# Optimization experiments

Measured on AMD Instinct MI355X. Metric: run time of the kernel, lower is better.

The kernel has to match this reference:

```python
import jax, jax.numpy as jnp
import numpy as np

N_NODES = 10000
N_EDGES = 320000
F_NODE = 16
NUM_BESSEL = 8
M = 32           # env_embed_multiplicity
LAT = 128        # latent dimension
R_MAX = 5.0
P_CUT = 6.0      # polynomial cutoff order
AVG_NEIGH = 32.0
SQRT3 = 1.7320508075688772
SQRT2 = 1.4142135623730951


def _mlp(x, weights):
    # nequip ScalarMLPFunction: linear layers with 1/sqrt(fan_in) norm, silu between layers
    h = x
    n = len(weights)
    for i, W in enumerate(weights):
        h = h @ W * (1.0 / np.sqrt(W.shape[0]))
        if i < n - 1:
            h = jax.nn.silu(h)
    return h


def _weight_channels(Y, w):
    # MakeWeightedChannels: Y [E,4] = (0e | 1e), w [E,M,2] per-irrep weights -> [E,M,4]
    return jnp.concatenate([w[..., 0:1] * Y[:, None, 0:1],
                            w[..., 1:2] * Y[:, None, 1:4]], axis=-1)


def setup_inputs():
    key = jax.random.key(0)
    ks = jax.random.split(key, 16)

    def w(k, i, o):
        return jax.random.normal(k, (i, o), jnp.float32)

    two_body_in = 2 * F_NODE + NUM_BESSEL  # 40
    return {
        "coordinates": jax.random.uniform(ks[0], (N_NODES, 3), jnp.float32),
        "node_attrs": jax.random.uniform(ks[1], (N_NODES, F_NODE), jnp.float32),
        "edge_index": jax.random.randint(ks[2], (2, N_EDGES), 0, N_NODES),
        "W2b0": w(ks[3], two_body_in, 64),
        "W2b1": w(ks[4], 64, 128),
        "W2b2": w(ks[5], 128, LAT),
        "Wenv0": w(ks[6], LAT, 4 * M),       # initial-edge embed + env weights (2 irreps each)
        "Wlat0": w(ks[7], LAT + 2 * M, 128),
        "Wlat1": w(ks[8], 128, LAT),
        "Ws0": w(ks[9], 2 * M, M),            # e3nn Linear, scalar block (2 paths)
        "Wv0": w(ks[10], 3 * M, M),           # e3nn Linear, vector block (3 paths)
        "Wenv1": w(ks[11], LAT, 2 * M),
        "Wfin0": w(ks[12], LAT + 2 * M, 128),
        "Wfin1": w(ks[13], 128, LAT),
    }


def reference(coordinates, node_attrs, edge_index, W2b0, W2b1, W2b2, Wenv0,
              Wlat0, Wlat1, Ws0, Wv0, Wenv1, Wfin0, Wfin1):
    sender, center = edge_index[0], edge_index[1]
    vec = coordinates[center] - coordinates[sender]            # [E,3]
    r = jnp.sqrt(jnp.sum(vec * vec, axis=-1) + 1e-12)          # [E]
    u = r / R_MAX
    p = P_CUT
    fcut = (1.0 - (p + 1.0) * (p + 2.0) / 2.0 * u**p
            + p * (p + 2.0) * u**(p + 1.0)
            - p * (p + 1.0) / 2.0 * u**(p + 2.0))
    fcut = jnp.where(u < 1.0, fcut, 0.0)
    n = jnp.arange(1, NUM_BESSEL + 1, dtype=jnp.float32)
    bessel = np.sqrt(2.0 / R_MAX) * jnp.sin(n * jnp.pi * u[:, None]) / r[:, None]
    edge_feats = bessel * fcut[:, None]                        # [E,8]
    unit = vec / r[:, None]
    Y = jnp.concatenate([jnp.ones_like(r)[:, None], SQRT3 * unit], axis=-1)  # [E,4] component-normalized SH

    inv_sqrt_n = 1.0 / np.sqrt(AVG_NEIGH)
    E = r.shape[0]

    # two-body latent (layer 0)
    lat_in = jnp.concatenate([node_attrs[center], node_attrs[sender], edge_feats], -1)
    lat = _mlp(lat_in, (W2b0, W2b1, W2b2)) * fcut[:, None]     # [E,LAT]
    w_all = lat @ Wenv0 * (1.0 / np.sqrt(LAT))                 # [E,4M]
    w_edge = w_all[:, :2 * M].reshape(E, M, 2)
    w_env = w_all[:, 2 * M:].reshape(E, M, 2)
    feat = _weight_channels(Y, w_edge)                         # [E,M,4] initial edge embed
    env = jax.ops.segment_sum(_weight_channels(Y, w_env), center, num_segments=N_NODES)
    env = env[center] * inv_sqrt_n                             # [E,M,4]

    fs, fv = feat[..., 0], feat[..., 1:]
    es, ev = env[..., 0], env[..., 1:]
    # layer-0 tensor product instruction list (uuu, no weights)
    p0 = fs * es                               # 0e x 0e -> 0e
    p1 = jnp.sum(fv * ev, -1) / SQRT3          # 1e x 1e -> 0e
    p2 = fs[..., None] * ev                    # 0e x 1e -> 1e
    p3 = fv * es[..., None]                    # 1e x 0e -> 1e
    p4 = jnp.cross(fv, ev) / SQRT2             # 1e x 1e -> 1e
    scal0 = jnp.concatenate([p0, p1], -1)      # [E,2M] scalar outs (n_scalar_outs=2)
    # per-layer e3nn Linear
    s_mix = scal0 @ Ws0 * (1.0 / np.sqrt(2 * M))                         # [E,M]
    v_mix = jnp.einsum('eic,io->eoc', jnp.concatenate([p2, p3, p4], 1), Wv0) * (1.0 / np.sqrt(3 * M))  # [E,M,3]

    # latent resnet update (update param 0 -> sigmoid = 0.5)
    alpha = 0.5
    c_old = 1.0 / np.sqrt(alpha * alpha + 1.0)
    c_new = alpha * c_old
    new_lat = _mlp(jnp.concatenate([lat, scal0], -1), (Wlat0, Wlat1)) * fcut[:, None]
    lat = c_old * lat + c_new * new_lat

    # layer 1 env embedding + tensor product (last layer -> scalars only)
    w_env1 = (lat @ Wenv1 * (1.0 / np.sqrt(LAT))).reshape(E, M, 2)
    env1 = jax.ops.segment_sum(_weight_channels(Y, w_env1), center, num_segments=N_NODES)
    env1 = env1[center] * inv_sqrt_n
    q0 = s_mix * env1[..., 0]
    q1 = jnp.sum(v_mix * env1[..., 1:], -1) / SQRT3
    scal1 = jnp.concatenate([q0, q1], -1)      # [E,2M]

    new_lat = _mlp(jnp.concatenate([lat, scal1], -1), (Wfin0, Wfin1)) * fcut[:, None]
    lat = c_old * lat + c_new * new_lat

    node_out = jax.ops.segment_sum(lat, center, num_segments=N_NODES) * inv_sqrt_n
    return node_out
```

## Files before the change

kernel.cpp:

```cpp
#include <hip/hip_runtime.h>
#include <hip/hip_bf16.h>
#include <math.h>

typedef __hip_bfloat16 bf16;
typedef unsigned short us;
typedef __attribute__((ext_vector_type(8))) short short8;
typedef __attribute__((ext_vector_type(4))) float floatx4;

#define EPI_SPLIT    1
#define EPI_STORE    2
#define EPI_RESID    4

#define INV_SQRT_N 0.17677669529663687f
#define INV_SQRT3  0.5773502691896258f
#define INV_SQRT2  0.7071067811865476f
#define C_OLD      0.8944271909999159f
#define C_NEW      0.4472135954999579f
#define PI_F       3.14159265358979323846f
#define SQRT3_F    1.7320508075688772f
#define BESSEL_PREF 0.6324555320336759f

__device__ __forceinline__ float b2f(bf16 x) { return __bfloat162float(x); }
__device__ __forceinline__ bf16  f2b(float x) { return __float2bfloat16(x); }
__device__ __forceinline__ us f2bu(float x) {
  bf16 h = f2b(x); us u; __builtin_memcpy(&u, &h, 2); return u;
}
__device__ __forceinline__ float silu_f(float v) { return v / (1.f + __expf(-v)); }
__device__ __forceinline__ floatx4 mfma16(short8 a, short8 b, floatx4 c) {
  return __builtin_amdgcn_mfma_f32_16x16x32_bf16(a, b, c, 0, 0, 0);
}
__device__ __forceinline__ short8 ld8(const void* p) {
  return *reinterpret_cast<const short8*>(p);
}
#define ZERO8 ((short8){0,0,0,0,0,0,0,0})

__global__ __launch_bounds__(256) void k_deg(
    const int* __restrict__ eidx, int E, int* __restrict__ deg) {
  int e = blockIdx.x * 256 + threadIdx.x;
  if (e < E) atomicAdd(&deg[eidx[E + e]], 1);
}

__global__ __launch_bounds__(1024) void k_scan(
    const int* __restrict__ deg, int N,
    int* __restrict__ rowptr, int* __restrict__ cursor) {
  __shared__ int part[1024];
  int t = threadIdx.x;
  int C = (N + 1023) / 1024;
  int base = t * C;
  int s = 0;
  for (int i = 0; i < C; ++i) { int idx = base + i; if (idx < N) s += deg[idx]; }
  part[t] = s;
  __syncthreads();
  for (int off = 1; off < 1024; off <<= 1) {
    int v = (t >= off) ? part[t - off] : 0;
    __syncthreads();
    part[t] += v;
    __syncthreads();
  }
  int excl = (t == 0) ? 0 : part[t - 1];
  for (int i = 0; i < C; ++i) {
    int idx = base + i;
    if (idx < N) { rowptr[idx] = excl; cursor[idx] = excl; excl += deg[idx]; }
  }
  if (t == 0) rowptr[N] = part[1023];
}

__global__ __launch_bounds__(256) void k_fill(
    const int* __restrict__ eidx, int E, int* __restrict__ cursor,
    int* __restrict__ eord, int* __restrict__ cent) {
  int e = blockIdx.x * 256 + threadIdx.x;
  if (e >= E) return;
  int c = eidx[E + e];
  int slot = atomicAdd(&cursor[c], 1);
  eord[slot] = e;
  cent[slot] = c;
}

__global__ __launch_bounds__(256) void k_geom(
    const float* __restrict__ coords, const float* __restrict__ nattr,
    const int* __restrict__ eidx, const int* __restrict__ eord, int E,
    float* __restrict__ fcut, float* __restrict__ Yb, bf16* __restrict__ a64) {
  int j = blockIdx.x * 256 + threadIdx.x;
  if (j >= E) return;
  int e = eord[j];
  int s = eidx[e], c = eidx[E + e];
  float dx = coords[c*3+0] - coords[s*3+0];
  float dy = coords[c*3+1] - coords[s*3+1];
  float dz = coords[c*3+2] - coords[s*3+2];
  float r = sqrtf(dx*dx + dy*dy + dz*dz + 1e-12f);
  float u = r * 0.2f;
  float u3 = u*u*u;
  float u6 = u3*u3, u7 = u6*u, u8 = u7*u;
  float fc = 1.f - 28.f*u6 + 48.f*u7 - 21.f*u8;
  fc = (u < 1.f) ? fc : 0.f;
  float inv_r = 1.f / r;
  fcut[j] = fc;
  Yb[j*4+0] = 1.f;
  Yb[j*4+1] = SQRT3_F * dx * inv_r;
  Yb[j*4+2] = SQRT3_F * dy * inv_r;
  Yb[j*4+3] = SQRT3_F * dz * inv_r;
  bf16* row = a64 + (long)j * 64;
  #pragma unroll
  for (int i = 0; i < 16; ++i) row[i]      = f2b(nattr[(long)c*16 + i]);
  #pragma unroll
  for (int i = 0; i < 16; ++i) row[16 + i] = f2b(nattr[(long)s*16 + i]);
  float pref = BESSEL_PREF * inv_r * fc;
  #pragma unroll
  for (int n = 1; n <= 8; ++n)
    row[32 + n - 1] = f2b(pref * sinf((float)n * PI_F * u));
  #pragma unroll
  for (int i = 40; i < 64; ++i) row[i] = f2b(0.f);
}

__device__ __forceinline__ void wp(const float* W, us* Wt, int K, int NOUT, int t) {
  int n = t / K, k = t % K;
  Wt[n * K + k] = f2bu(W[k * NOUT + n]);
}

__global__ __launch_bounds__(256) void k_wprep_all(
    const float* W2b0, const float* W2b1, const float* W2b2,
    const float* Wenv0, const float* Wlat0, const float* Wlat1,
    const float* Wenv1, const float* Wfin0, const float* Wfin1,
    const float* Ws0, const float* Wv0,
    us* W2b0p, us* W2b1t, us* W2b2t, us* Wenv0t, us* Wlat0t, us* Wlat1t,
    us* Wenv1t, us* Wfin0t, us* Wfin1t, us* Wmixt) {
  int t = blockIdx.x * 256 + threadIdx.x;
  if (t < 8192)  { wp(W2b1,  W2b1t,  64, 128, t); return; } t -= 8192;
  if (t < 16384) { wp(W2b2,  W2b2t, 128, 128, t); return; } t -= 16384;
  if (t < 16384) { wp(Wenv0, Wenv0t,128, 128, t); return; } t -= 16384;
  if (t < 24576) { wp(Wlat0, Wlat0t,192, 128, t); return; } t -= 24576;
  if (t < 16384) { wp(Wlat1, Wlat1t,128, 128, t); return; } t -= 16384;
  if (t < 8192)  { wp(Wenv1, Wenv1t,128,  64, t); return; } t -= 8192;
  if (t < 24576) { wp(Wfin0, Wfin0t,192, 128, t); return; } t -= 24576;
  if (t < 16384) { wp(Wfin1, Wfin1t,128, 128, t); return; } t -= 16384;
  if (t < 4096)  {
    int n = t >> 6, k = t & 63;
    W2b0p[n * 64 + k] = (k < 40) ? f2bu(W2b0[k * 64 + n]) : 0;
    return;
  } t -= 4096;
  if (t < 5120) {
    int o = t / 160, k = t % 160;
    float v = (k < 64) ? Ws0[k * 32 + o] : Wv0[(k - 64) * 32 + o];
    Wmixt[o * 160 + k] = f2bu(v);
  }
}

__global__ __launch_bounds__(256) void k_envg(
    const bf16* __restrict__ wenv, const float* __restrict__ Yb,
    const int* __restrict__ rowptr, int N, float* __restrict__ env) {
  int t = blockIdx.x * 256 + threadIdx.x;
  if (t >= N * 32) return;
  int n = t >> 5, m = t & 31;
  int j0 = rowptr[n], j1 = rowptr[n + 1];
  float a0 = 0.f, a1 = 0.f, a2 = 0.f, a3 = 0.f;
  for (int j = j0; j < j1; ++j) {
    float w0 = b2f(wenv[(long)j*64 + 2*m]);
    float w1 = b2f(wenv[(long)j*64 + 2*m + 1]);
    float4 y = *reinterpret_cast<const float4*>(&Yb[(long)j*4]);
    a0 += w0;
    a1 += w1 * y.y;
    a2 += w1 * y.z;
    a3 += w1 * y.w;
  }
  *reinterpret_cast<float4*>(&env[(long)n*128 + m*4]) = make_float4(a0, a1, a2, a3);
}

__global__ __launch_bounds__(256) void k_nodeg(
    const bf16* __restrict__ lat, const int* __restrict__ rowptr,
    int N, float* __restrict__ out) {
  int t = blockIdx.x * 256 + threadIdx.x;
  if (t >= N * 128) return;
  int n = t >> 7, j = t & 127;
  int j0 = rowptr[n], j1 = rowptr[n + 1];
  float s = 0.f;
  for (int q = j0; q < j1; ++q)
    s += b2f(lat[(long)q*128 + j]);
  out[t] = s * INV_SQRT_N;
}

template<int NOUT, int EPI>
__global__ __launch_bounds__(256) void mgemm(
    const bf16* __restrict__ A, const us* __restrict__ Wt,
    bf16* __restrict__ out1, bf16* __restrict__ out2, float scale, int E) {
  constexpr int K = 128, KP = 136, NC = 4;
  constexpr int CT = NOUT / 64;
  __shared__ __align__(16) us As[64 * KP];
  int tid = threadIdx.x;
  int lane = tid & 63, w = tid >> 6;
  int nl = lane & 15, quad = lane >> 4;
  long e0 = (long)blockIdx.x * 64;

  short8 wf[NC][CT];
  #pragma unroll
  for (int kc = 0; kc < NC; ++kc)
    #pragma unroll
    for (int ct = 0; ct < CT; ++ct)
      wf[kc][ct] = ld8(Wt + (long)(w*CT*16 + ct*16 + nl) * K + kc*32 + quad*8);

  #pragma unroll
  for (int it = 0; it < 4; ++it) {
    int i = tid + it * 256;
    int row = i >> 4, col = (i & 15) * 8;
    long eg = e0 + row;
    short8 v = (eg < E) ? ld8(A + eg * 128 + col) : ZERO8;
    *(short8*)&As[row * KP + col] = v;
  }
  __syncthreads();

  floatx4 acc[4][CT];
  #pragma unroll
  for (int i = 0; i < 4; ++i)
    #pragma unroll
    for (int j = 0; j < CT; ++j) acc[i][j] = (floatx4){0.f,0.f,0.f,0.f};
  #pragma unroll
  for (int kc = 0; kc < NC; ++kc) {
    short8 af[4];
    #pragma unroll
    for (int et = 0; et < 4; ++et)
      af[et] = ld8(&As[(et*16 + nl) * KP + kc*32 + quad*8]);
    #pragma unroll
    for (int et = 0; et < 4; ++et)
      #pragma unroll
      for (int ct = 0; ct < CT; ++ct)
        acc[et][ct] = mfma16(af[et], wf[kc][ct], acc[et][ct]);
  }

  #pragma unroll
  for (int et = 0; et < 4; ++et)
    #pragma unroll
    for (int ct = 0; ct < CT; ++ct)
      #pragma unroll
      for (int r = 0; r < 4; ++r) {
        long eg = e0 + et*16 + quad*4 + r;
        if (eg >= E) continue;
        int col = w*CT*16 + ct*16 + nl;
        float v = acc[et][ct][r] * scale;
        if constexpr (EPI == EPI_SPLIT) {
          if (col < 64) out1[eg * 64 + col] = f2b(v);
          else          out2[eg * 64 + (col - 64)] = f2b(v);
        } else {
          out1[eg * NOUT + col] = f2b(v);
        }
      }
}

__global__ __launch_bounds__(256) void mfused3(
    const bf16* __restrict__ a64, const us* __restrict__ W0p,
    const us* __restrict__ W1t, const us* __restrict__ W2t,
    bf16* __restrict__ lat, const float* __restrict__ fcut,
    float s40, float s64s, float s128, int E) {
  constexpr int AP = 72, HP = 136;
  __shared__ __align__(16) us SB[64 * 144];
  us* As = SB;
  us* H0 = SB + 64 * AP;
  us* Hs = SB;
  int tid = threadIdx.x;
  int lane = tid & 63, w = tid >> 6;
  int nl = lane & 15, quad = lane >> 4;
  long e0 = (long)blockIdx.x * 64;

  short8 w0f[2], w1f[2][2], w2f[4][2];
  #pragma unroll
  for (int kc = 0; kc < 2; ++kc)
    w0f[kc] = ld8(W0p + (w*16 + nl) * 64 + kc*32 + quad*8);
  #pragma unroll
  for (int kc = 0; kc < 2; ++kc)
    #pragma unroll
    for (int ct = 0; ct < 2; ++ct)
      w1f[kc][ct] = ld8(W1t + (long)(w*32 + ct*16 + nl) * 64 + kc*32 + quad*8);
  #pragma unroll
  for (int kc = 0; kc < 4; ++kc)
    #pragma unroll
    for (int ct = 0; ct < 2; ++ct)
      w2f[kc][ct] = ld8(W2t + (long)(w*32 + ct*16 + nl) * 128 + kc*32 + quad*8);

  #pragma unroll
  for (int it = 0; it < 2; ++it) {
    int i = tid + it * 256;
    int row = i >> 3, col = (i & 7) * 8;
    long eg = e0 + row;
    short8 v = (eg < E) ? ld8(a64 + eg * 64 + col) : ZERO8;
    *(short8*)&As[row * AP + col] = v;
  }
  __syncthreads();

  floatx4 a0[4];
  #pragma unroll
  for (int i = 0; i < 4; ++i) a0[i] = (floatx4){0.f,0.f,0.f,0.f};
  #pragma unroll
  for (int kc = 0; kc < 2; ++kc) {
    short8 af[4];
    #pragma unroll
    for (int et = 0; et < 4; ++et)
      af[et] = ld8(&As[(et*16 + nl) * AP + kc*32 + quad*8]);
    #pragma unroll
    for (int et = 0; et < 4; ++et) a0[et] = mfma16(af[et], w0f[kc], a0[et]);
  }
  #pragma unroll
  for (int et = 0; et < 4; ++et)
    #pragma unroll
    for (int r = 0; r < 4; ++r)
      H0[(et*16 + quad*4 + r) * AP + w*16 + nl] = f2bu(silu_f(a0[et][r] * s40));
  __syncthreads();

  floatx4 acc[4][2];
  #pragma unroll
  for (int i = 0; i < 4; ++i)
    #pragma unroll
    for (int j = 0; j < 2; ++j) acc[i][j] = (floatx4){0.f,0.f,0.f,0.f};
  #pragma unroll
  for (int kc = 0; kc < 2; ++kc) {
    short8 af[4];
    #pragma unroll
    for (int et = 0; et < 4; ++et)
      af[et] = ld8(&H0[(et*16 + nl) * AP + kc*32 + quad*8]);
    #pragma unroll
    for (int et = 0; et < 4; ++et)
      #pragma unroll
      for (int ct = 0; ct < 2; ++ct)
        acc[et][ct] = mfma16(af[et], w1f[kc][ct], acc[et][ct]);
  }
  __syncthreads();

  #pragma unroll
  for (int et = 0; et < 4; ++et)
    #pragma unroll
    for (int ct = 0; ct < 2; ++ct)
      #pragma unroll
      for (int r = 0; r < 4; ++r)
        Hs[(et*16 + quad*4 + r) * HP + w*32 + ct*16 + nl] =
            f2bu(silu_f(acc[et][ct][r] * s64s));
  __syncthreads();

  #pragma unroll
  for (int i = 0; i < 4; ++i)
    #pragma unroll
    for (int j = 0; j < 2; ++j) acc[i][j] = (floatx4){0.f,0.f,0.f,0.f};
  #pragma unroll
  for (int kc = 0; kc < 4; ++kc) {
    short8 af[4];
    #pragma unroll
    for (int et = 0; et < 4; ++et)
      af[et] = ld8(&Hs[(et*16 + nl) * HP + kc*32 + quad*8]);
    #pragma unroll
    for (int et = 0; et < 4; ++et)
      #pragma unroll
      for (int ct = 0; ct < 2; ++ct)
        acc[et][ct] = mfma16(af[et], w2f[kc][ct], acc[et][ct]);
  }
  #pragma unroll
  for (int et = 0; et < 4; ++et)
    #pragma unroll
    for (int ct = 0; ct < 2; ++ct)
      #pragma unroll
      for (int r = 0; r < 4; ++r) {
        long eg = e0 + et*16 + quad*4 + r;
        if (eg >= E) continue;
        lat[eg * 128 + w*32 + ct*16 + nl] =
            f2b(acc[et][ct][r] * s128 * fcut[eg]);
      }
}

template<int EPI>
__global__ __launch_bounds__(256) void mfused(
    const bf16* __restrict__ A, const bf16* __restrict__ A2,
    const us* __restrict__ W0t, const us* __restrict__ W1t,
    bf16* __restrict__ outb, const float* __restrict__ fcut,
    float scale0, float scale1, int E) {
  constexpr int K = 192, KP = 200, NC0 = 6, HP = 136;
  __shared__ __align__(16) us SB[64 * KP];
  us* As = SB;
  us* Hs = SB;
  int tid = threadIdx.x;
  int lane = tid & 63, w = tid >> 6;
  int nl = lane & 15, quad = lane >> 4;
  long e0 = (long)blockIdx.x * 64;

  short8 w0f[NC0][2];
  #pragma unroll
  for (int kc = 0; kc < NC0; ++kc)
    #pragma unroll
    for (int ct = 0; ct < 2; ++ct)
      w0f[kc][ct] = ld8(W0t + (long)(w*32 + ct*16 + nl) * K + kc*32 + quad*8);

  #pragma unroll
  for (int it = 0; it < 4; ++it) {
    int i = tid + it * 256;
    int row = i >> 4, col = (i & 15) * 8;
    long eg = e0 + row;
    short8 v = (eg < E) ? ld8(A + eg * 128 + col) : ZERO8;
    *(short8*)&As[row * KP + col] = v;
  }
  #pragma unroll
  for (int it = 0; it < 2; ++it) {
    int i = tid + it * 256;
    int row = i >> 3, col = (i & 7) * 8;
    long eg = e0 + row;
    short8 v = (eg < E) ? ld8(A2 + eg * 64 + col) : ZERO8;
    *(short8*)&As[row * KP + 128 + col] = v;
  }
  __syncthreads();

  floatx4 acc[4][2];
  #pragma unroll
  for (int i = 0; i < 4; ++i)
    #pragma unroll
    for (int j = 0; j < 2; ++j) acc[i][j] = (floatx4){0.f,0.f,0.f,0.f};
  #pragma unroll
  for (int kc = 0; kc < NC0; ++kc) {
    short8 af[4];
    #pragma unroll
    for (int et = 0; et < 4; ++et)
      af[et] = ld8(&As[(et*16 + nl) * KP + kc*32 + quad*8]);
    #pragma unroll
    for (int et = 0; et < 4; ++et)
      #pragma unroll
      for (int ct = 0; ct < 2; ++ct)
        acc[et][ct] = mfma16(af[et], w0f[kc][ct], acc[et][ct]);
  }

  short8 w1f[4][2];
  #pragma unroll
  for (int kc = 0; kc < 4; ++kc)
    #pragma unroll
    for (int ct = 0; ct < 2; ++ct)
      w1f[kc][ct] = ld8(W1t + (long)(w*32 + ct*16 + nl) * 128 + kc*32 + quad*8);

  __syncthreads();

  #pragma unroll
  for (int et = 0; et < 4; ++et)
    #pragma unroll
    for (int ct = 0; ct < 2; ++ct)
      #pragma unroll
      for (int r = 0; r < 4; ++r)
        Hs[(et*16 + quad*4 + r) * HP + w*32 + ct*16 + nl] =
            f2bu(silu_f(acc[et][ct][r] * scale0));
  __syncthreads();

  #pragma unroll
  for (int i = 0; i < 4; ++i)
    #pragma unroll
    for (int j = 0; j < 2; ++j) acc[i][j] = (floatx4){0.f,0.f,0.f,0.f};
  #pragma unroll
  for (int kc = 0; kc < 4; ++kc) {
    short8 af[4];
    #pragma unroll
    for (int et = 0; et < 4; ++et)
      af[et] = ld8(&Hs[(et*16 + nl) * HP + kc*32 + quad*8]);
    #pragma unroll
    for (int et = 0; et < 4; ++et)
      #pragma unroll
      for (int ct = 0; ct < 2; ++ct)
        acc[et][ct] = mfma16(af[et], w1f[kc][ct], acc[et][ct]);
  }

  #pragma unroll
  for (int et = 0; et < 4; ++et)
    #pragma unroll
    for (int ct = 0; ct < 2; ++ct)
      #pragma unroll
      for (int r = 0; r < 4; ++r) {
        long eg = e0 + et*16 + quad*4 + r;
        if (eg >= E) continue;
        int col = w*32 + ct*16 + nl;
        float v = acc[et][ct][r] * scale1 * fcut[eg];
        long idx = eg * 128 + col;
        outb[idx] = f2b(C_OLD * b2f(outb[idx]) + C_NEW * v);
      }
}

__global__ __launch_bounds__(256) void k_prod(
    const bf16* __restrict__ wedge, const float* __restrict__ env,
    const float* __restrict__ Yb, const int* __restrict__ cent, int E,
    bf16* __restrict__ scal) {
  long t = (long)blockIdx.x * 256 + threadIdx.x;
  if (t >= (long)E * 32) return;
  long e = t >> 5;
  int m = (int)(t & 31);
  int c = cent[e];
  float w0 = b2f(wedge[e*64 + 2*m]), w1 = b2f(wedge[e*64 + 2*m + 1]);
  const float* ep = env + (long)c*128 + m*4;
  float es  = ep[0] * INV_SQRT_N;
  float evx = ep[1] * INV_SQRT_N, evy = ep[2] * INV_SQRT_N, evz = ep[3] * INV_SQRT_N;
  float y1 = Yb[e*4+1], y2 = Yb[e*4+2], y3 = Yb[e*4+3];
  float fvx = w1*y1, fvy = w1*y2, fvz = w1*y3;
  scal[e*64 + m]      = f2b(w0 * es);
  scal[e*64 + 32 + m] = f2b((fvx*evx + fvy*evy + fvz*evz) * INV_SQRT3);
}

__global__ __launch_bounds__(256) void k_mix2(
    const bf16* __restrict__ wedge, const float* __restrict__ env,
    const float* __restrict__ env1, const float* __restrict__ Yb,
    const int* __restrict__ cent, const us* __restrict__ Wm,
    int E, bf16* __restrict__ scal) {
  constexpr int PP = 360;
  constexpr int RP = 132;
  __shared__ __align__(16) unsigned char SB[64 * PP * 2];
  __shared__ __align__(16) us Wl[32 * 160];
  us* P = (us*)SB;
  float* R = (float*)SB;
  int tid = threadIdx.x;
  int lane = tid & 63, w = tid >> 6;
  int nl = lane & 15, quad = lane >> 4;
  long e0 = (long)blockIdx.x * 64;

  for (int i = tid; i < 640; i += 256)
    *(short8*)&Wl[i * 8] = ld8(Wm + i * 8);

  int m = tid & 31;
  #pragma unroll
  for (int it = 0; it < 8; ++it) {
    int el = (tid >> 5) + it * 8;
    long e = e0 + el;
    if (e < E) {
      int c = cent[e];
      float w0 = b2f(wedge[e*64 + 2*m]), w1 = b2f(wedge[e*64 + 2*m + 1]);
      float4 ev4 = *(const float4*)(env + (long)c*128 + m*4);
      float4 y   = *(const float4*)(Yb + e*4);
      float es  = ev4.x * INV_SQRT_N;
      float evx = ev4.y * INV_SQRT_N, evy = ev4.z * INV_SQRT_N, evz = ev4.w * INV_SQRT_N;
      float fvx = w1*y.y, fvy = w1*y.z, fvz = w1*y.w;
      us* p = P + el * PP;
      p[m]       = f2bu(w0 * es);
      p[32 + m]  = f2bu((fvx*evx + fvy*evy + fvz*evz) * INV_SQRT3);
      p[64 + m]  = f2bu(w0 * evx);
      p[96 + m]  = f2bu(fvx * es);
      p[128 + m] = f2bu((fvy*evz - fvz*evy) * INV_SQRT2);
      p[160 + m] = f2bu(w0 * evy);
      p[192 + m] = f2bu(fvy * es);
      p[224 + m] = f2bu((fvz*evx - fvx*evz) * INV_SQRT2);
      p[256 + m] = f2bu(w0 * evz);
      p[288 + m] = f2bu(fvz * es);
      p[320 + m] = f2bu((fvx*evy - fvy*evx) * INV_SQRT2);
    } else {
      us* p = P + el * PP;
      #pragma unroll
      for (int q = 0; q < 11; ++q) p[q*32 + m] = 0;
    }
  }
  __syncthreads();

  floatx4 acc[4][2];
  #pragma unroll
  for (int i = 0; i < 4; ++i)
    #pragma unroll
    for (int j = 0; j < 2; ++j) acc[i][j] = (floatx4){0.f,0.f,0.f,0.f};
  int pbase  = (w == 0) ? 0 : 64 + (w - 1) * 96;
  int wkbase = (w == 0) ? 0 : 64;
  int ksteps = (w == 0) ? 2 : 3;
  for (int ks = 0; ks < ksteps; ++ks) {
    short8 af[4], bv[2];
    #pragma unroll
    for (int et = 0; et < 4; ++et)
      af[et] = ld8(&P[(et*16 + nl) * PP + pbase + ks*32 + quad*8]);
    #pragma unroll
    for (int ct = 0; ct < 2; ++ct)
      bv[ct] = ld8(&Wl[(ct*16 + nl) * 160 + wkbase + ks*32 + quad*8]);
    #pragma unroll
    for (int et = 0; et < 4; ++et)
      #pragma unroll
      for (int ct = 0; ct < 2; ++ct)
        acc[et][ct] = mfma16(af[et], bv[ct], acc[et][ct]);
  }
  __syncthreads();

  #pragma unroll
  for (int et = 0; et < 4; ++et)
    #pragma unroll
    for (int ct = 0; ct < 2; ++ct)
      #pragma unroll
      for (int r = 0; r < 4; ++r) {
        int el = et*16 + quad*4 + r;
        R[el * RP + w*32 + ct*16 + nl] = acc[et][ct][r];
      }
  __syncthreads();

  #pragma unroll
  for (int it = 0; it < 8; ++it) {
    int el = (tid >> 5) + it * 8;
    long e = e0 + el;
    if (e >= E) continue;
    int o = m;
    int c = cent[e];
    float4 e1 = *(const float4*)(env1 + (long)c*128 + o*4);
    float sr = R[el * RP + o];
    float vx = R[el * RP + 32 + o];
    float vy = R[el * RP + 64 + o];
    float vz = R[el * RP + 96 + o];
    float q0 = sr * 0.125f * (e1.x * INV_SQRT_N);
    float q1 = (vx*e1.y + vy*e1.z + vz*e1.w) *
               (0.10206207261596577f * INV_SQRT_N * INV_SQRT3);
    scal[e*64 + o]      = f2b(q0);
    scal[e*64 + 32 + o] = f2b(q1);
  }
}

extern "C" void kernel_launch(void* const* d_in, const int* in_sizes, int n_in,
                              void* d_out, int out_size, void* d_ws, size_t ws_size,
                              hipStream_t stream) {
  const float* coords = (const float*)d_in[0];
  const float* nattr  = (const float*)d_in[1];
  const int*   eidx   = (const int*)d_in[2];
  const float* W2b0   = (const float*)d_in[3];
  const float* W2b1   = (const float*)d_in[4];
  const float* W2b2   = (const float*)d_in[5];
  const float* Wenv0  = (const float*)d_in[6];
  const float* Wlat0  = (const float*)d_in[7];
  const float* Wlat1  = (const float*)d_in[8];
  const float* Ws0    = (const float*)d_in[9];
  const float* Wv0    = (const float*)d_in[10];
  const float* Wenv1  = (const float*)d_in[11];
  const float* Wfin0  = (const float*)d_in[12];
  const float* Wfin1  = (const float*)d_in[13];
  float* out = (float*)d_out;
  int E = in_sizes[2] / 2;
  int N = in_sizes[0] / 3;

  float* fcut   = (float*)d_ws;
  float* Yb     = fcut + (size_t)E;
  float* env    = Yb + (size_t)E*4;
  float* env1   = env + (size_t)N*128;
  int*   deg    = (int*)(env1 + (size_t)N*128);
  int*   rowptr = deg + N;
  int*   cursor = rowptr + (N + 8);
  int*   eord   = cursor + N;
  int*   cent   = eord + E;
  bf16*  b64    = (bf16*)(cent + E);
  bf16*  lat    = b64 + (size_t)E*64;
  bf16*  S      = lat + (size_t)E*128;
  us* W2b1t  = (us*)(S + (size_t)E*64);
  us* W2b2t  = W2b1t + 128*64;
  us* Wenv0t = W2b2t + 128*128;
  us* Wlat0t = Wenv0t + 128*128;
  us* Wlat1t = Wlat0t + 128*192;
  us* Wenv1t = Wlat1t + 128*128;
  us* Wfin0t = Wenv1t + 64*128;
  us* Wfin1t = Wfin0t + 128*192;
  us* W2b0p  = Wfin1t + 128*128;
  us* Wmixt  = W2b0p + 64*64;

  hipMemsetAsync(deg, 0, (size_t)N * sizeof(int), stream);

  dim3 blk(256);
  const float s40  = 0.15811388300841897f;
  const float s64  = 0.125f;
  const float s128 = 0.08838834764831845f;
  const float s192 = 0.07216878364870323f;
  int gB = (E + 63) / 64;
  int gE = (E + 255) / 256;

  k_deg<<<gE, blk, 0, stream>>>(eidx, E, deg);
  k_scan<<<1, 1024, 0, stream>>>(deg, N, rowptr, cursor);
  k_fill<<<gE, blk, 0, stream>>>(eidx, E, cursor, eord, cent);
  k_geom<<<gE, blk, 0, stream>>>(coords, nattr, eidx, eord, E, fcut, Yb, S );
  k_wprep_all<<<dim3(548), blk, 0, stream>>>(
      W2b0, W2b1, W2b2, Wenv0, Wlat0, Wlat1, Wenv1, Wfin0, Wfin1, Ws0, Wv0,
      W2b0p, W2b1t, W2b2t, Wenv0t, Wlat0t, Wlat1t, Wenv1t, Wfin0t, Wfin1t, Wmixt);

  mfused3<<<gB, blk, 0, stream>>>(
      S , W2b0p, W2b1t, W2b2t, lat, fcut, s40, s64, s128, E);

  mgemm<128,EPI_SPLIT><<<gB, blk, 0, stream>>>(
      lat, Wenv0t, b64, S , s128, E);

  k_envg<<<dim3((N*32 + 255) / 256), blk, 0, stream>>>(
      S , Yb, rowptr, N, env);

  k_prod<<<dim3((int)(((long)E*32 + 255) / 256)), blk, 0, stream>>>(
      b64, env, Yb, cent, E, S );

  mfused<EPI_RESID><<<gB, blk, 0, stream>>>(
      lat, S , Wlat0t, Wlat1t, lat, fcut, s192, s128, E);

  mgemm<64,EPI_STORE><<<gB, blk, 0, stream>>>(
      lat, Wenv1t, S , nullptr, s128, E);

  k_envg<<<dim3((N*32 + 255) / 256), blk, 0, stream>>>(
      S , Yb, rowptr, N, env1);

  k_mix2<<<gB, blk, 0, stream>>>(
      b64, env, env1, Yb, cent, Wmixt, E, S );

  mfused<EPI_RESID><<<gB, blk, 0, stream>>>(
      lat, S , Wfin0t, Wfin1t, lat, fcut, s192, s128, E);

  k_nodeg<<<dim3((N*128 + 255) / 256), blk, 0, stream>>>(
      lat, rowptr, N, out);
}
```

Baseline: 771.5 us.

## Fuse env-weight GEMMs into MLP kernels and env gather with product

Folds the Wenv0 projection into the two-body MLP kernel and the Wenv1 projection into the first latent-update kernel. The freshly computed latent tile is staged in shared memory and multiplied in place, so the separate GEMM kernels and their re-read of the latent array go away. The env gather and the per-edge product are merged into one node-ordered kernel that computes the product right after the segment sum. This removes the scattered cent-indexed env reads and two launches, at the cost of extra register pressure, extra syncs and a serial per-node loop in the merged gather.

```diff
diff --git a/kernel.cpp b/kernel.cpp
--- a/kernel.cpp
+++ b/kernel.cpp
@@ -6,10 +6,6 @@
 typedef unsigned short us;
 typedef __attribute__((ext_vector_type(8))) short short8;
 typedef __attribute__((ext_vector_type(4))) float floatx4;
-
-#define EPI_SPLIT    1
-#define EPI_STORE    2
-#define EPI_RESID    4
 
 #define INV_SQRT_N 0.17677669529663687f
 #define INV_SQRT3  0.5773502691896258f
@@ -24,6 +20,9 @@
 __device__ __forceinline__ bf16  f2b(float x) { return __float2bfloat16(x); }
 __device__ __forceinline__ us f2bu(float x) {
   bf16 h = f2b(x); us u; __builtin_memcpy(&u, &h, 2); return u;
+}
+__device__ __forceinline__ float bu2f(us u) {
+  bf16 h; __builtin_memcpy(&h, &u, 2); return b2f(h);
 }
 __device__ __forceinline__ float silu_f(float v) { return v / (1.f + __expf(-v)); }
 __device__ __forceinline__ floatx4 mfma16(short8 a, short8 b, floatx4 c) {
@@ -145,6 +144,37 @@
   }
 }
 
+__global__ __launch_bounds__(256) void k_envgp(
+    const bf16* __restrict__ wenv, const bf16* __restrict__ wedge,
+    const float* __restrict__ Yb, const int* __restrict__ rowptr,
+    int N, float* __restrict__ env, bf16* __restrict__ scal) {
+  int t = blockIdx.x * 256 + threadIdx.x;
+  if (t >= N * 32) return;
+  int n = t >> 5, m = t & 31;
+  int j0 = rowptr[n], j1 = rowptr[n + 1];
+  float a0 = 0.f, a1 = 0.f, a2 = 0.f, a3 = 0.f;
+  for (int j = j0; j < j1; ++j) {
+    float w0 = b2f(wenv[(long)j*64 + 2*m]);
+    float w1 = b2f(wenv[(long)j*64 + 2*m + 1]);
+    float4 y = *reinterpret_cast<const float4*>(&Yb[(long)j*4]);
+    a0 += w0;
+    a1 += w1 * y.y;
+    a2 += w1 * y.z;
+    a3 += w1 * y.w;
+  }
+  *reinterpret_cast<float4*>(&env[(long)n*128 + m*4]) = make_float4(a0, a1, a2, a3);
+  float es  = a0 * INV_SQRT_N;
+  float evx = a1 * INV_SQRT_N, evy = a2 * INV_SQRT_N, evz = a3 * INV_SQRT_N;
+  for (int j = j0; j < j1; ++j) {
+    float w0 = b2f(wedge[(long)j*64 + 2*m]);
+    float w1 = b2f(wedge[(long)j*64 + 2*m + 1]);
+    float4 y = *reinterpret_cast<const float4*>(&Yb[(long)j*4]);
+    float fvx = w1*y.y, fvy = w1*y.z, fvz = w1*y.w;
+    scal[(long)j*64 + m]      = f2b(w0 * es);
+    scal[(long)j*64 + 32 + m] = f2b((fvx*evx + fvy*evy + fvz*evz) * INV_SQRT3);
+  }
+}
+
 __global__ __launch_bounds__(256) void k_envg(
     const bf16* __restrict__ wenv, const float* __restrict__ Yb,
     const int* __restrict__ rowptr, int N, float* __restrict__ env) {
@@ -178,76 +208,12 @@
   out[t] = s * INV_SQRT_N;
 }
 
-template<int NOUT, int EPI>
-__global__ __launch_bounds__(256) void mgemm(
-    const bf16* __restrict__ A, const us* __restrict__ Wt,
-    bf16* __restrict__ out1, bf16* __restrict__ out2, float scale, int E) {
-  constexpr int K = 128, KP = 136, NC = 4;
-  constexpr int CT = NOUT / 64;
-  __shared__ __align__(16) us As[64 * KP];
-  int tid = threadIdx.x;
-  int lane = tid & 63, w = tid >> 6;
-  int nl = lane & 15, quad = lane >> 4;
-  long e0 = (long)blockIdx.x * 64;
-
-  short8 wf[NC][CT];
-  #pragma unroll
-  for (int kc = 0; kc < NC; ++kc)
-    #pragma unroll
-    for (int ct = 0; ct < CT; ++ct)
-      wf[kc][ct] = ld8(Wt + (long)(w*CT*16 + ct*16 + nl) * K + kc*32 + quad*8);
-
-  #pragma unroll
-  for (int it = 0; it < 4; ++it) {
-    int i = tid + it * 256;
-    int row = i >> 4, col = (i & 15) * 8;
-    long eg = e0 + row;
-    short8 v = (eg < E) ? ld8(A + eg * 128 + col) : ZERO8;
-    *(short8*)&As[row * KP + col] = v;
-  }
-  __syncthreads();
-
-  floatx4 acc[4][CT];
-  #pragma unroll
-  for (int i = 0; i < 4; ++i)
-    #pragma unroll
-    for (int j = 0; j < CT; ++j) acc[i][j] = (floatx4){0.f,0.f,0.f,0.f};
-  #pragma unroll
-  for (int kc = 0; kc < NC; ++kc) {
-    short8 af[4];
-    #pragma unroll
-    for (int et = 0; et < 4; ++et)
-      af[et] = ld8(&As[(et*16 + nl) * KP + kc*32 + quad*8]);
-    #pragma unroll
-    for (int et = 0; et < 4; ++et)
-      #pragma unroll
-      for (int ct = 0; ct < CT; ++ct)
-        acc[et][ct] = mfma16(af[et], wf[kc][ct], acc[et][ct]);
-  }
-
-  #pragma unroll
-  for (int et = 0; et < 4; ++et)
-    #pragma unroll
-    for (int ct = 0; ct < CT; ++ct)
-      #pragma unroll
-      for (int r = 0; r < 4; ++r) {
-        long eg = e0 + et*16 + quad*4 + r;
-        if (eg >= E) continue;
-        int col = w*CT*16 + ct*16 + nl;
-        float v = acc[et][ct][r] * scale;
-        if constexpr (EPI == EPI_SPLIT) {
-          if (col < 64) out1[eg * 64 + col] = f2b(v);
-          else          out2[eg * 64 + (col - 64)] = f2b(v);
-        } else {
-          out1[eg * NOUT + col] = f2b(v);
-        }
-      }
-}
-
-__global__ __launch_bounds__(256) void mfused3(
+__global__ __launch_bounds__(256) void mfused3s(
     const bf16* __restrict__ a64, const us* __restrict__ W0p,
     const us* __restrict__ W1t, const us* __restrict__ W2t,
-    bf16* __restrict__ lat, const float* __restrict__ fcut,
+    const us* __restrict__ Wenv0t,
+    bf16* __restrict__ lat, bf16* __restrict__ b64, bf16* __restrict__ wenv,
+    const float* __restrict__ fcut,
     float s40, float s64s, float s128, int E) {
   constexpr int AP = 72, HP = 136;
   __shared__ __align__(16) us SB[64 * 144];
@@ -348,6 +314,49 @@
       for (int ct = 0; ct < 2; ++ct)
         acc[et][ct] = mfma16(af[et], w2f[kc][ct], acc[et][ct]);
   }
+
+  short8 wef[4][2];
+  #pragma unroll
+  for (int kc = 0; kc < 4; ++kc)
+    #pragma unroll
+    for (int ct = 0; ct < 2; ++ct)
+      wef[kc][ct] = ld8(Wenv0t + (long)(w*32 + ct*16 + nl) * 128 + kc*32 + quad*8);
+
+  __syncthreads();
+
+  #pragma unroll
+  for (int et = 0; et < 4; ++et)
+    #pragma unroll
+    for (int ct = 0; ct < 2; ++ct)
+      #pragma unroll
+      for (int r = 0; r < 4; ++r) {
+        long eg = e0 + et*16 + quad*4 + r;
+        int col = w*32 + ct*16 + nl;
+        us lv = 0;
+        if (eg < E) {
+          lv = f2bu(acc[et][ct][r] * s128 * fcut[eg]);
+          lat[eg * 128 + col] = f2b(bu2f(lv));
+        }
+        Hs[(et*16 + quad*4 + r) * HP + col] = lv;
+      }
+  __syncthreads();
+
+  #pragma unroll
+  for (int i = 0; i < 4; ++i)
+    #pragma unroll
+    for (int j = 0; j < 2; ++j) acc[i][j] = (floatx4){0.f,0.f,0.f,0.f};
+  #pragma unroll
+  for (int kc = 0; kc < 4; ++kc) {
+    short8 af[4];
+    #pragma unroll
+    for (int et = 0; et < 4; ++et)
+      af[et] = ld8(&Hs[(et*16 + nl) * HP + kc*32 + quad*8]);
+    #pragma unroll
+    for (int et = 0; et < 4; ++et)
+      #pragma unroll
+      for (int ct = 0; ct < 2; ++ct)
+        acc[et][ct] = mfma16(af[et], wef[kc][ct], acc[et][ct]);
+  }
   #pragma unroll
   for (int et = 0; et < 4; ++et)
     #pragma unroll
@@ -356,16 +365,20 @@
       for (int r = 0; r < 4; ++r) {
         long eg = e0 + et*16 + quad*4 + r;
         if (eg >= E) continue;
-        lat[eg * 128 + w*32 + ct*16 + nl] =
-            f2b(acc[et][ct][r] * s128 * fcut[eg]);
+        int col = w*32 + ct*16 + nl;
+        float v = acc[et][ct][r] * s128;
+        if (col < 64) b64[eg * 64 + col] = f2b(v);
+        else          wenv[eg * 64 + (col - 64)] = f2b(v);
       }
 }
 
-template<int EPI>
-__global__ __launch_bounds__(256) void mfused(
+template<int HAS_TAIL>
+__global__ __launch_bounds__(256) void mfuseds(
     const bf16* __restrict__ A, const bf16* __restrict__ A2,
     const us* __restrict__ W0t, const us* __restrict__ W1t,
-    bf16* __restrict__ outb, const float* __restrict__ fcut,
+    const us* __restrict__ Wenv1t,
+    bf16* __restrict__ outb, bf16* __restrict__ wenv1,
+    const float* __restrict__ fcut,
     float scale0, float scale1, int E) {
   constexpr int K = 192, KP = 200, NC0 = 6, HP = 136;
   __shared__ __align__(16) us SB[64 * KP];
@@ -455,38 +468,69 @@
         acc[et][ct] = mfma16(af[et], w1f[kc][ct], acc[et][ct]);
   }
 
-  #pragma unroll
-  for (int et = 0; et < 4; ++et)
-    #pragma unroll
-    for (int ct = 0; ct < 2; ++ct)
+  if constexpr (!HAS_TAIL) {
+    #pragma unroll
+    for (int et = 0; et < 4; ++et)
+      #pragma unroll
+      for (int ct = 0; ct < 2; ++ct)
+        #pragma unroll
+        for (int r = 0; r < 4; ++r) {
+          long eg = e0 + et*16 + quad*4 + r;
+          if (eg >= E) continue;
+          int col = w*32 + ct*16 + nl;
+          float v = acc[et][ct][r] * scale1 * fcut[eg];
+          long idx = eg * 128 + col;
+          outb[idx] = f2b(C_OLD * b2f(outb[idx]) + C_NEW * v);
+        }
+  } else {
+    short8 wef[4];
+    #pragma unroll
+    for (int kc = 0; kc < 4; ++kc)
+      wef[kc] = ld8(Wenv1t + (long)(w*16 + nl) * 128 + kc*32 + quad*8);
+
+    __syncthreads();
+
+    #pragma unroll
+    for (int et = 0; et < 4; ++et)
+      #pragma unroll
+      for (int ct = 0; ct < 2; ++ct)
+        #pragma unroll
+        for (int r = 0; r < 4; ++r) {
+          long eg = e0 + et*16 + quad*4 + r;
+          int col = w*32 + ct*16 + nl;
+          us lv = 0;
+          if (eg < E) {
+            float v = acc[et][ct][r] * scale1 * fcut[eg];
+            long idx = eg * 128 + col;
+            lv = f2bu(C_OLD * b2f(outb[idx]) + C_NEW * v);
+            outb[idx] = f2b(bu2f(lv));
+          }
+          Hs[(et*16 + quad*4 + r) * HP + col] = lv;
+        }
+    __syncthreads();
+
+    floatx4 acc2[4];
+    #pragma unroll
+    for (int i = 0; i < 4; ++i) acc2[i] = (floatx4){0.f,0.f,0.f,0.f};
+    #pragma unroll
+    for (int kc = 0; kc < 4; ++kc) {
+      short8 af[4];
+      #pragma unroll
+      for (int et = 0; et < 4; ++et)
+        af[et] = ld8(&Hs[(et*16 + nl) * HP + kc*32 + quad*8]);
+      #pragma unroll
+      for (int et = 0; et < 4; ++et)
+        acc2[et] = mfma16(af[et], wef[kc], acc2[et]);
+    }
+    #pragma unroll
+    for (int et = 0; et < 4; ++et)
       #pragma unroll
       for (int r = 0; r < 4; ++r) {
         long eg = e0 + et*16 + quad*4 + r;
         if (eg >= E) continue;
-        int col = w*32 + ct*16 + nl;
-        float v = acc[et][ct][r] * scale1 * fcut[eg];
-        long idx = eg * 128 + col;
-        outb[idx] = f2b(C_OLD * b2f(outb[idx]) + C_NEW * v);
+        wenv1[eg * 64 + w*16 + nl] = f2b(acc2[et][r] * 0.08838834764831845f);
       }
-}
-
-__global__ __launch_bounds__(256) void k_prod(
-    const bf16* __restrict__ wedge, const float* __restrict__ env,
-    const float* __restrict__ Yb, const int* __restrict__ cent, int E,
-    bf16* __restrict__ scal) {
-  long t = (long)blockIdx.x * 256 + threadIdx.x;
-  if (t >= (long)E * 32) return;
-  long e = t >> 5;
-  int m = (int)(t & 31);
-  int c = cent[e];
-  float w0 = b2f(wedge[e*64 + 2*m]), w1 = b2f(wedge[e*64 + 2*m + 1]);
-  const float* ep = env + (long)c*128 + m*4;
-  float es  = ep[0] * INV_SQRT_N;
-  float evx = ep[1] * INV_SQRT_N, evy = ep[2] * INV_SQRT_N, evz = ep[3] * INV_SQRT_N;
-  float y1 = Yb[e*4+1], y2 = Yb[e*4+2], y3 = Yb[e*4+3];
-  float fvx = w1*y1, fvy = w1*y2, fvz = w1*y3;
-  scal[e*64 + m]      = f2b(w0 * es);
-  scal[e*64 + 32 + m] = f2b((fvx*evx + fvy*evy + fvz*evz) * INV_SQRT3);
+  }
 }
 
 __global__ __launch_bounds__(256) void k_mix2(
@@ -658,23 +702,16 @@
       W2b0, W2b1, W2b2, Wenv0, Wlat0, Wlat1, Wenv1, Wfin0, Wfin1, Ws0, Wv0,
       W2b0p, W2b1t, W2b2t, Wenv0t, Wlat0t, Wlat1t, Wenv1t, Wfin0t, Wfin1t, Wmixt);
 
-  mfused3<<<gB, blk, 0, stream>>>(
-      S , W2b0p, W2b1t, W2b2t, lat, fcut, s40, s64, s128, E);
-
-  mgemm<128,EPI_SPLIT><<<gB, blk, 0, stream>>>(
-      lat, Wenv0t, b64, S , s128, E);
-
-  k_envg<<<dim3((N*32 + 255) / 256), blk, 0, stream>>>(
-      S , Yb, rowptr, N, env);
-
-  k_prod<<<dim3((int)(((long)E*32 + 255) / 256)), blk, 0, stream>>>(
-      b64, env, Yb, cent, E, S );
-
-  mfused<EPI_RESID><<<gB, blk, 0, stream>>>(
-      lat, S , Wlat0t, Wlat1t, lat, fcut, s192, s128, E);
-
-  mgemm<64,EPI_STORE><<<gB, blk, 0, stream>>>(
-      lat, Wenv1t, S , nullptr, s128, E);
+  mfused3s<<<gB, blk, 0, stream>>>(
+      S , W2b0p, W2b1t, W2b2t, Wenv0t, lat, b64, S , fcut,
+      s40, s64, s128, E);
+
+  k_envgp<<<dim3((N*32 + 255) / 256), blk, 0, stream>>>(
+      S , b64, Yb, rowptr, N, env, S );
+
+  mfuseds<1><<<gB, blk, 0, stream>>>(
+      lat, S , Wlat0t, Wlat1t, Wenv1t, lat, S , fcut,
+      s192, s128, E);
 
   k_envg<<<dim3((N*32 + 255) / 256), blk, 0, stream>>>(
       S , Yb, rowptr, N, env1);
@@ -682,8 +719,9 @@
   k_mix2<<<gB, blk, 0, stream>>>(
       b64, env, env1, Yb, cent, Wmixt, E, S );
 
-  mfused<EPI_RESID><<<gB, blk, 0, stream>>>(
-      lat, S , Wfin0t, Wfin1t, lat, fcut, s192, s128, E);
+  mfuseds<0><<<gB, blk, 0, stream>>>(
+      lat, S , Wfin0t, Wfin1t, nullptr, lat, nullptr, fcut,
+      s192, s128, E);
 
   k_nodeg<<<dim3((N*128 + 255) / 256), blk, 0, stream>>>(
       lat, rowptr, N, out);
```

Measured after the change: 722.7 us. 6.3% less time.
